# Optimization experiments

Hardware: AMD Instinct MI355X
Metric: run time of the kernel (lower is better)

Reference implementation:

```python
import jax, jax.numpy as jnp
import numpy as np
from jax import lax

HIDDEN = 256
HORIZON = 168  # 7 * 24


def _cell(x, h, c, Wih, Whh, bih, bhh):
    # PyTorch LSTM cell: gate order i, f, g, o
    gates = x @ Wih.T + bih + h @ Whh.T + bhh  # [B, 4*HIDDEN]
    i, f, g, o = jnp.split(gates, 4, axis=-1)
    c = jax.nn.sigmoid(f) * c + jax.nn.sigmoid(i) * jnp.tanh(g)
    h = jax.nn.sigmoid(o) * jnp.tanh(c)
    return h, c


def setup_inputs() -> dict:
    key = jax.random.key(0)
    ks = jax.random.split(key, 20)
    B, T, H = 1024, 336, HIDDEN
    s = 0.05

    def p(k, shape):
        return jax.random.normal(k, shape, dtype=jnp.float32) * s

    inp = {"x": jax.random.normal(ks[0], (B, T), dtype=jnp.float32)}
    # encoder layer 0 (input_size=1), layer 1 (input=HIDDEN)
    inp["enc_Wih0"] = p(ks[1], (4 * H, 1)); inp["enc_Whh0"] = p(ks[2], (4 * H, H))
    inp["enc_bih0"] = p(ks[3], (4 * H,)); inp["enc_bhh0"] = p(ks[4], (4 * H,))
    inp["enc_Wih1"] = p(ks[5], (4 * H, H)); inp["enc_Whh1"] = p(ks[6], (4 * H, H))
    inp["enc_bih1"] = p(ks[7], (4 * H,)); inp["enc_bhh1"] = p(ks[8], (4 * H,))
    # decoder layers
    inp["dec_Wih0"] = p(ks[9], (4 * H, 1)); inp["dec_Whh0"] = p(ks[10], (4 * H, H))
    inp["dec_bih0"] = p(ks[11], (4 * H,)); inp["dec_bhh0"] = p(ks[12], (4 * H,))
    inp["dec_Wih1"] = p(ks[13], (4 * H, H)); inp["dec_Whh1"] = p(ks[14], (4 * H, H))
    inp["dec_bih1"] = p(ks[15], (4 * H,)); inp["dec_bhh1"] = p(ks[16], (4 * H,))
    # final projection hidden -> 1
    inp["fc_W"] = p(ks[17], (1, H)); inp["fc_b"] = p(ks[18], (1,))
    return inp


def reference(x, enc_Wih0, enc_Whh0, enc_bih0, enc_bhh0,
              enc_Wih1, enc_Whh1, enc_bih1, enc_bhh1,
              dec_Wih0, dec_Whh0, dec_bih0, dec_bhh0,
              dec_Wih1, dec_Whh1, dec_bih1, dec_bhh1,
              fc_W, fc_b):
    B = x.shape[0]
    xs = x[:, :, None].transpose(1, 0, 2)  # [T, B, 1]
    z = jnp.zeros((B, HIDDEN), dtype=x.dtype)

    def enc_step(carry, xt):
        h0, c0, h1, c1 = carry
        h0, c0 = _cell(xt, h0, c0, enc_Wih0, enc_Whh0, enc_bih0, enc_bhh0)
        h1, c1 = _cell(h0, h1, c1, enc_Wih1, enc_Whh1, enc_bih1, enc_bhh1)
        return (h0, c0, h1, c1), None

    (h0, c0, h1, c1), _ = lax.scan(enc_step, (z, z, z, z), xs)

    dec_inp = x[:, -1:]  # [B, 1] last observed value

    def dec_step(carry, _):
        h0, c0, h1, c1, inp = carry
        h0, c0 = _cell(inp, h0, c0, dec_Wih0, dec_Whh0, dec_bih0, dec_bhh0)
        h1, c1 = _cell(h0, h1, c1, dec_Wih1, dec_Whh1, dec_bih1, dec_bhh1)
        pred = h1 @ fc_W.T + fc_b  # [B, 1]
        return (h0, c0, h1, c1, pred), pred

    _, preds = lax.scan(dec_step, (h0, c0, h1, c1, dec_inp), None, length=HORIZON)
    return preds[:, :, 0].T  # [B, HORIZON]
```

## Files before the change

### kernel.cpp

```cpp
#include <hip/hip_runtime.h>

#define HIDDEN 256
#define TENC 336
#define HORIZ 168
#define BSZ 1024
#define BH (BSZ*HIDDEN)
#define WMAT (1024*256)

typedef _Float16 f16;
typedef f16 f16x8 __attribute__((ext_vector_type(8)));
typedef float f32x4 __attribute__((ext_vector_type(4)));
typedef unsigned int u32;
typedef unsigned long long u64;

#define H0_OFF 0
#define H1_OFF (2*BH*2)
#define PP_OFF (H1_OFF + 2*BH*2)
#define FLAG_OFF (PP_OFF + BSZ*16*4)
#define WS_BASE (FLAG_OFF + 16*16*64)
#define WF16_OFF WS_BASE
#define WS_FULL (WF16_OFF + 6*WMAT*2)

#define LDS_A0 0
#define LDS_A1 32768
#define LDS_X0 65536
#define XSTRIDE 16
#define LDS_X1 (LDS_X0 + 256*XSTRIDE*4)
#define LDS_SM (LDS_X1 + 256*XSTRIDE*4)
#define LDS_TOTAL (LDS_SM + 1024)

__device__ __forceinline__ float sigm(float x){ return 1.0f/(1.0f+__expf(-x)); }
__device__ __forceinline__ float tanh_f(float x){ return 2.0f/(1.0f+__expf(-2.0f*x)) - 1.0f; }

__device__ __forceinline__ u64 ald64(const void* p){
  return __hip_atomic_load((const u64*)p, __ATOMIC_RELAXED, __HIP_MEMORY_SCOPE_AGENT);
}
__device__ __forceinline__ u32 ald32(const u32* p){
  return __hip_atomic_load(p, __ATOMIC_RELAXED, __HIP_MEMORY_SCOPE_AGENT);
}
__device__ __forceinline__ void ast32(u32* p, u32 v){
  __hip_atomic_store(p, v, __ATOMIC_RELAXED, __HIP_MEMORY_SCOPE_AGENT);
}

__device__ __forceinline__ f16x8 loadWfrag(const float* W, int grow, int k){
  const float* p = W + grow*HIDDEN + k;
  float4 lo = *(const float4*)p;
  float4 hi = *(const float4*)(p+4);
  f16x8 r;
  r[0]=(f16)lo.x; r[1]=(f16)lo.y; r[2]=(f16)lo.z; r[3]=(f16)lo.w;
  r[4]=(f16)hi.x; r[5]=(f16)hi.y; r[6]=(f16)hi.z; r[7]=(f16)hi.w;
  return r;
}

__device__ __forceinline__ const f16* slot_src(const f16* base, int g, int s){
  int l = s & 63, f = s >> 6;
  int kt = f >> 2, mt = f & 3;
  int row = g*64 + mt*16 + (l&15);
  int k = kt*32 + 8*(l>>4);
  return base + row*HIDDEN + k;
}

__device__ __forceinline__ void stage_tile(char* dst, const f16* src_base, int g, int tid){
  u64 v[8];
  #pragma unroll
  for (int i=0;i<4;++i){
    const f16* src = slot_src(src_base, g, tid + 512*i);
    v[2*i]   = ald64(src);
    v[2*i+1] = ald64(src+4);
  }
  #pragma unroll
  for (int i=0;i<4;++i){
    int s = tid + 512*i;
    *(u64*)(dst + s*16)     = v[2*i];
    *(u64*)(dst + s*16 + 8) = v[2*i+1];
  }
}

__device__ __forceinline__ void stage2(char* dA, const f16* sA, char* dB, const f16* sB,
                                       int g, int tid){
  u64 va[8], vb[8];
  #pragma unroll
  for (int i=0;i<4;++i){
    const f16* src = slot_src(sA, g, tid + 512*i);
    va[2*i]   = ald64(src);
    va[2*i+1] = ald64(src+4);
  }
  #pragma unroll
  for (int i=0;i<4;++i){
    const f16* src = slot_src(sB, g, tid + 512*i);
    vb[2*i]   = ald64(src);
    vb[2*i+1] = ald64(src+4);
  }
  #pragma unroll
  for (int i=0;i<4;++i){
    int s = tid + 512*i;
    *(u64*)(dA + s*16)     = va[2*i];
    *(u64*)(dA + s*16 + 8) = va[2*i+1];
    *(u64*)(dB + s*16)     = vb[2*i];
    *(u64*)(dB + s*16 + 8) = vb[2*i+1];
  }
}

__device__ __forceinline__ void cellpair(const float* X, const float* bs, const float* wih, float xr,
                                         int crow, int dp, float& ca, float& cb, float& hA, float& hB){
  float iA = X[(0*64+crow)*XSTRIDE+dp  ] + bs[dp]      + xr*wih[dp];
  float iB = X[(0*64+crow)*XSTRIDE+dp+1] + bs[dp+1]    + xr*wih[dp+1];
  float fA = X[(1*64+crow)*XSTRIDE+dp  ] + bs[16+dp]   + xr*wih[16+dp];
  float fB = X[(1*64+crow)*XSTRIDE+dp+1] + bs[16+dp+1] + xr*wih[16+dp+1];
  float gA = X[(2*64+crow)*XSTRIDE+dp  ] + bs[32+dp]   + xr*wih[32+dp];
  float gB = X[(2*64+crow)*XSTRIDE+dp+1] + bs[32+dp+1] + xr*wih[32+dp+1];
  float oA = X[(3*64+crow)*XSTRIDE+dp  ] + bs[48+dp]   + xr*wih[48+dp];
  float oB = X[(3*64+crow)*XSTRIDE+dp+1] + bs[48+dp+1] + xr*wih[48+dp+1];
  ca = sigm(fA)*ca + sigm(iA)*tanh_f(gA);
  cb = sigm(fB)*cb + sigm(iB)*tanh_f(gB);
  hA = sigm(oA)*tanh_f(ca);
  hB = sigm(oB)*tanh_f(cb);
}

__device__ __forceinline__ void storeh(f16* base, int rowg, int col, float hA, float hB){
  u32 pk = (u32)__builtin_bit_cast(unsigned short, (f16)hA)
         | ((u32)__builtin_bit_cast(unsigned short, (f16)hB) << 16);
  ast32((u32*)(base + rowg*HIDDEN + col), pk);
}

__device__ __forceinline__ void gbar(u32* gf, int j, int lane, int tid, u32 ev){
  __syncthreads();
  if (tid == 0) ast32(gf + j*16, ev);
  if (tid < 64 && lane < 16){
    const u32* sp = gf + lane*16;
    for (int it = 0; it < (1<<17); ++it){
      if (__all((int)(ald32(sp) >= ev))) break;
    }
  }
  __syncthreads();
}

struct P {
  const float *x;
  const float *eWih0,*eWhh0,*eBih0,*eBhh0,*eWih1,*eWhh1,*eBih1,*eBhh1;
  const float *dWih0,*dWhh0,*dBih0,*dBhh0,*dWih1,*dWhh1,*dBih1,*dBhh1;
  const float *fcW,*fcB;
  float* out;
  char* ws;
  int usef16;
};

struct WC {
  const float* src0; const float* src1; const float* src2;
  const float* src3; const float* src4; const float* src5;
  f16* dst;
};

__global__ void initk(char* ws){
  u32* p = (u32*)ws;
  size_t total = (size_t)WS_BASE / 4;
  for (size_t k = (size_t)blockIdx.x*blockDim.x + threadIdx.x; k < total;
       k += (size_t)gridDim.x*blockDim.x) p[k] = 0u;
}

__global__ void wconv(WC wc){
  int m = blockIdx.y;
  const float* s = (m==0)?wc.src0:(m==1)?wc.src1:(m==2)?wc.src2:
                   (m==3)?wc.src3:(m==4)?wc.src4:wc.src5;
  f16* d = wc.dst + (size_t)m*WMAT;
  for (int i = blockIdx.x*blockDim.x + threadIdx.x; i < WMAT;
       i += gridDim.x*blockDim.x) d[i] = (f16)s[i];
}

__global__ __launch_bounds__(512) void lstm_main(P p){
  const int tid  = threadIdx.x;
  const int lane = tid & 63;
  const int w    = tid >> 6;
  const int n    = w & 3;
  const int mh   = w >> 2;
  const int blk  = blockIdx.x;
  const int g    = blk & 15;
  const int j    = blk >> 4;

  extern __shared__ __align__(16) char smem[];
  char*  A0 = smem + LDS_A0;
  char*  A1 = smem + LDS_A1;
  float* X0 = (float*)(smem + LDS_X0);
  float* X1 = (float*)(smem + LDS_X1);
  float* wih0s = (float*)(smem + LDS_SM);
  float* b0s   = wih0s + 64;
  float* b1s   = wih0s + 128;
  float* fcWs  = wih0s + 192;
  float* fcbs  = wih0s + 208;

  f16*   h0buf = (f16*)(p.ws + H0_OFF);
  f16*   h1buf = (f16*)(p.ws + H1_OFF);
  float* ppart = (float*)(p.ws + PP_OFF);
  u32*   gf    = (u32*)(p.ws + FLAG_OFF) + g*256;
  const f16* wf = (const f16*)(p.ws + WF16_OFF);

  const int crow = tid >> 3;
  const int dp   = (tid & 7) * 2;
  const int rowg = g*64 + crow;
  const int cold = j*16 + dp;

  float c0a=0.f, c0b=0.f, c1a=0.f, c1b=0.f;

  if (tid < 64){
    int gt = tid >> 4, d = tid & 15;
    int grow = gt*256 + j*16 + d;
    wih0s[tid] = p.eWih0[grow];
    b0s[tid] = p.eBih0[grow] + p.eBhh0[grow];
    b1s[tid] = p.eBih1[grow] + p.eBhh1[grow];
  }
  if (tid < 16) fcWs[tid] = p.fcW[j*16 + tid];
  if (tid == 0) fcbs[0] = p.fcB[0];

  const int grow = n*256 + j*16 + (lane & 15);
  const int kb = 8*(lane>>4);
  f16x8 B0[8], B1i[8], B1h[8];
  if (p.usef16){
    #pragma unroll
    for (int kt=0; kt<8; ++kt){
      int ko = kt*32 + kb;
      B0[kt]  = *(const f16x8*)(wf + 0*WMAT + grow*HIDDEN + ko);
      B1i[kt] = *(const f16x8*)(wf + 1*WMAT + grow*HIDDEN + ko);
      B1h[kt] = *(const f16x8*)(wf + 2*WMAT + grow*HIDDEN + ko);
    }
  } else {
    #pragma unroll
    for (int kt=0; kt<8; ++kt){
      B0[kt]  = loadWfrag(p.eWhh0, grow, kt*32 + kb);
      B1i[kt] = loadWfrag(p.eWih1, grow, kt*32 + kb);
      B1h[kt] = loadWfrag(p.eWhh1, grow, kt*32 + kb);
    }
  }
  __syncthreads();

  u32 ev = 0;

  for (int r = 0; r <= TENC; ++r){
    float xr = (r < TENC) ? p.x[rowg*TENC + r] : 0.f;
    stage2(A0, h0buf + ((r+1)&1)*BH, A1, h1buf + (r&1)*BH, g, tid);
    __syncthreads();

    f32x4 acc0[2] = {{0.f,0.f,0.f,0.f},{0.f,0.f,0.f,0.f}};
    f32x4 acc1[2] = {{0.f,0.f,0.f,0.f},{0.f,0.f,0.f,0.f}};
    #pragma unroll
    for (int kt=0; kt<8; ++kt){
      #pragma unroll
      for (int m=0; m<2; ++m){
        f16x8 a = *(const f16x8*)(A0 + ((kt*4 + (mh*2+m))*64 + lane)*16);
        acc0[m] = __builtin_amdgcn_mfma_f32_16x16x32_f16(a, B0[kt],  acc0[m], 0,0,0);
        acc1[m] = __builtin_amdgcn_mfma_f32_16x16x32_f16(a, B1i[kt], acc1[m], 0,0,0);
      }
    }
    #pragma unroll
    for (int kt=0; kt<8; ++kt){
      #pragma unroll
      for (int m=0; m<2; ++m){
        f16x8 a = *(const f16x8*)(A1 + ((kt*4 + (mh*2+m))*64 + lane)*16);
        acc1[m] = __builtin_amdgcn_mfma_f32_16x16x32_f16(a, B1h[kt], acc1[m], 0,0,0);
      }
    }

    #pragma unroll
    for (int m=0; m<2; ++m){
      int rb = mh*32 + m*16 + 4*(lane>>4);
      #pragma unroll
      for (int q=0; q<4; ++q){
        X0[(n*64 + rb + q)*XSTRIDE + (lane&15)] = acc0[m][q];
        X1[(n*64 + rb + q)*XSTRIDE + (lane&15)] = acc1[m][q];
      }
    }
    __syncthreads();

    if (r < TENC){
      float hA, hB;
      cellpair(X0, b0s, wih0s, xr, crow, dp, c0a, c0b, hA, hB);
      storeh(h0buf + (r&1)*BH, rowg, cold, hA, hB);
    }
    if (r >= 1){
      float hA, hB;
      cellpair(X1, b1s, wih0s, 0.f, crow, dp, c1a, c1b, hA, hB);
      storeh(h1buf + ((r-1)&1)*BH, rowg, cold, hA, hB);
    }
    ++ev;
    gbar(gf, j, lane, tid, ev);
  }

  __syncthreads();
  if (tid < 64){
    int gt = tid >> 4, d = tid & 15;
    int grw = gt*256 + j*16 + d;
    wih0s[tid] = p.dWih0[grw];
    b0s[tid] = p.dBih0[grw] + p.dBhh0[grw];
    b1s[tid] = p.dBih1[grw] + p.dBhh1[grw];
  }
  if (p.usef16){
    #pragma unroll
    for (int kt=0; kt<8; ++kt){
      int ko = kt*32 + kb;
      B0[kt]  = *(const f16x8*)(wf + 3*WMAT + grow*HIDDEN + ko);
      B1i[kt] = *(const f16x8*)(wf + 4*WMAT + grow*HIDDEN + ko);
      B1h[kt] = *(const f16x8*)(wf + 5*WMAT + grow*HIDDEN + ko);
    }
  } else {
    #pragma unroll
    for (int kt=0; kt<8; ++kt){
      B0[kt]  = loadWfrag(p.dWhh0, grow, kt*32 + kb);
      B1i[kt] = loadWfrag(p.dWih1, grow, kt*32 + kb);
      B1h[kt] = loadWfrag(p.dWhh1, grow, kt*32 + kb);
    }
  }
  __syncthreads();

  for (int t = 0; t < HORIZ; ++t){
    u64 ppv = 0;
    float xlast = 0.f;
    if (t == 0) xlast = p.x[rowg*TENC + (TENC-1)];
    else        ppv   = ald64(ppart + rowg*16 + (tid&7)*2);

    stage2(A0, h0buf + ((t+1)&1)*BH, A1, h1buf + ((t+1)&1)*BH, g, tid);
    __syncthreads();

    f32x4 acc0[2] = {{0.f,0.f,0.f,0.f},{0.f,0.f,0.f,0.f}};
    f32x4 acc1[2] = {{0.f,0.f,0.f,0.f},{0.f,0.f,0.f,0.f}};
    #pragma unroll
    for (int kt=0; kt<8; ++kt){
      #pragma unroll
      for (int m=0; m<2; ++m){
        f16x8 a0 = *(const f16x8*)(A0 + ((kt*4 + (mh*2+m))*64 + lane)*16);
        acc0[m] = __builtin_amdgcn_mfma_f32_16x16x32_f16(a0, B0[kt],  acc0[m], 0,0,0);
        f16x8 a1 = *(const f16x8*)(A1 + ((kt*4 + (mh*2+m))*64 + lane)*16);
        acc1[m] = __builtin_amdgcn_mfma_f32_16x16x32_f16(a1, B1h[kt], acc1[m], 0,0,0);
      }
    }
    #pragma unroll
    for (int m=0; m<2; ++m){
      int rb = mh*32 + m*16 + 4*(lane>>4);
      #pragma unroll
      for (int q=0; q<4; ++q) X0[(n*64 + rb + q)*XSTRIDE + (lane&15)] = acc0[m][q];
    }
    __syncthreads();

    float inp;
    if (t == 0){
      inp = xlast;
    } else {
      float a = __builtin_bit_cast(float, (u32)(ppv & 0xffffffffull));
      float b = __builtin_bit_cast(float, (u32)(ppv >> 32));
      float s = a + b;
      s += __shfl_xor(s, 1);
      s += __shfl_xor(s, 2);
      s += __shfl_xor(s, 4);
      inp = s + fcbs[0];
    }
    {
      float hA, hB;
      cellpair(X0, b0s, wih0s, inp, crow, dp, c0a, c0b, hA, hB);
      storeh(h0buf + (t&1)*BH, rowg, cold, hA, hB);
    }
    if (t > 0 && j == 0 && (tid & 7) == 0) p.out[rowg*HORIZ + (t-1)] = inp;
    ++ev;
    gbar(gf, j, lane, tid, ev);

    stage_tile(A0, h0buf + (t&1)*BH, g, tid);
    __syncthreads();

    #pragma unroll
    for (int kt=0; kt<8; ++kt){
      #pragma unroll
      for (int m=0; m<2; ++m){
        f16x8 a0 = *(const f16x8*)(A0 + ((kt*4 + (mh*2+m))*64 + lane)*16);
        acc1[m] = __builtin_amdgcn_mfma_f32_16x16x32_f16(a0, B1i[kt], acc1[m], 0,0,0);
      }
    }
    #pragma unroll
    for (int m=0; m<2; ++m){
      int rb = mh*32 + m*16 + 4*(lane>>4);
      #pragma unroll
      for (int q=0; q<4; ++q) X1[(n*64 + rb + q)*XSTRIDE + (lane&15)] = acc1[m][q];
    }
    __syncthreads();

    {
      float hA, hB;
      cellpair(X1, b1s, wih0s, 0.f, crow, dp, c1a, c1b, hA, hB);
      storeh(h1buf + (t&1)*BH, rowg, cold, hA, hB);
      float pp = fcWs[dp]*hA + fcWs[dp+1]*hB;
      pp += __shfl_xor(pp, 1);
      pp += __shfl_xor(pp, 2);
      pp += __shfl_xor(pp, 4);
      if ((tid & 7) == 0)
        ast32((u32*)(ppart + rowg*16 + j), __builtin_bit_cast(u32, pp));
    }
    ++ev;
    gbar(gf, j, lane, tid, ev);
  }

  if (j == 0){
    u64 ppv = ald64(ppart + rowg*16 + (tid&7)*2);
    float a = __builtin_bit_cast(float, (u32)(ppv & 0xffffffffull));
    float b = __builtin_bit_cast(float, (u32)(ppv >> 32));
    float s = a + b;
    s += __shfl_xor(s, 1);
    s += __shfl_xor(s, 2);
    s += __shfl_xor(s, 4);
    if ((tid & 7) == 0) p.out[rowg*HORIZ + (HORIZ-1)] = s + fcbs[0];
  }
}

extern "C" void kernel_launch(void* const* d_in, const int* in_sizes, int n_in,
                              void* d_out, int out_size, void* d_ws, size_t ws_size,
                              hipStream_t stream) {
  (void)in_sizes; (void)n_in; (void)out_size;
  if (ws_size < (size_t)WS_BASE) return;
  const int usef16 = (ws_size >= (size_t)WS_FULL) ? 1 : 0;

  P prm;
  prm.x     = (const float*)d_in[0];
  prm.eWih0 = (const float*)d_in[1];  prm.eWhh0 = (const float*)d_in[2];
  prm.eBih0 = (const float*)d_in[3];  prm.eBhh0 = (const float*)d_in[4];
  prm.eWih1 = (const float*)d_in[5];  prm.eWhh1 = (const float*)d_in[6];
  prm.eBih1 = (const float*)d_in[7];  prm.eBhh1 = (const float*)d_in[8];
  prm.dWih0 = (const float*)d_in[9];  prm.dWhh0 = (const float*)d_in[10];
  prm.dBih0 = (const float*)d_in[11]; prm.dBhh0 = (const float*)d_in[12];
  prm.dWih1 = (const float*)d_in[13]; prm.dWhh1 = (const float*)d_in[14];
  prm.dBih1 = (const float*)d_in[15]; prm.dBhh1 = (const float*)d_in[16];
  prm.fcW   = (const float*)d_in[17]; prm.fcB   = (const float*)d_in[18];
  prm.out   = (float*)d_out;
  prm.ws    = (char*)d_ws;
  prm.usef16 = usef16;

  hipLaunchKernelGGL(initk, dim3(256), dim3(256), 0, stream, (char*)d_ws);

  if (usef16){
    WC wc;
    wc.src0 = prm.eWhh0; wc.src1 = prm.eWih1; wc.src2 = prm.eWhh1;
    wc.src3 = prm.dWhh0; wc.src4 = prm.dWih1; wc.src5 = prm.dWhh1;
    wc.dst  = (f16*)((char*)d_ws + WF16_OFF);
    hipLaunchKernelGGL(wconv, dim3(128, 6), dim3(256), 0, stream, wc);
  }

  hipFuncSetAttribute((const void*)lstm_main,
                      hipFuncAttributeMaxDynamicSharedMemorySize, LDS_TOTAL);
  void* args[] = { &prm };
  hipLaunchCooperativeKernel((const void*)lstm_main, dim3(256), dim3(512),
                             args, LDS_TOTAL, stream);
}
```

Before: 4.385 ms.

## Split group barrier into per-layer flag signals to overlap layer pipelines

Replaces the single per-group barrier with two flag arrays, one for layer-0 and one for layer-1 hidden-state readiness, each signalled and polled separately. In the encoder, a block can start layer-0 work as soon as the previous layer-0 states are published, without waiting on layer-1 completion, which lets the two layers' stages skew and overlap across blocks. In exchange there are more polling points per step and subtler ordering requirements (flag counts, WAR hazards on double-buffered h) that could cause races if any dependency is missing. The poll timeout is raised.

```diff
diff --git a/kernel.cpp b/kernel.cpp
--- a/kernel.cpp
+++ b/kernel.cpp
@@ -17,7 +17,7 @@
 #define H1_OFF (2*BH*2)
 #define PP_OFF (H1_OFF + 2*BH*2)
 #define FLAG_OFF (PP_OFF + BSZ*16*4)
-#define WS_BASE (FLAG_OFF + 16*16*64)
+#define WS_BASE (FLAG_OFF + 16*32*64)
 #define WF16_OFF WS_BASE
 #define WS_FULL (WF16_OFF + 6*WMAT*2)
 
@@ -123,16 +123,22 @@
   ast32((u32*)(base + rowg*HIDDEN + col), pk);
 }
 
-__device__ __forceinline__ void gbar(u32* gf, int j, int lane, int tid, u32 ev){
+__device__ __forceinline__ void pollw(const u32* f0, u32 t0, const u32* f1, u32 t1, int tid){
+  if (tid < 64){
+    const u32* sp = nullptr; u32 tgt = 0;
+    if (tid < 16){ sp = f0 + tid*16; tgt = t0; }
+    else if (f1 != nullptr && tid < 32){ sp = f1 + (tid-16)*16; tgt = t1; }
+    for (int it = 0; it < (1<<20); ++it){
+      bool ok = (sp == nullptr) || (ald32(sp) >= tgt);
+      if (__all((int)ok)) break;
+    }
+  }
   __syncthreads();
-  if (tid == 0) ast32(gf + j*16, ev);
-  if (tid < 64 && lane < 16){
-    const u32* sp = gf + lane*16;
-    for (int it = 0; it < (1<<17); ++it){
-      if (__all((int)(ald32(sp) >= ev))) break;
-    }
-  }
+}
+
+__device__ __forceinline__ void sigf(u32* line, u32 v, int tid){
   __syncthreads();
+  if (tid == 0) ast32(line, v);
 }
 
 struct P {
@@ -191,8 +197,11 @@
   f16*   h0buf = (f16*)(p.ws + H0_OFF);
   f16*   h1buf = (f16*)(p.ws + H1_OFF);
   float* ppart = (float*)(p.ws + PP_OFF);
-  u32*   gf    = (u32*)(p.ws + FLAG_OFF) + g*256;
-  const f16* wf = (const f16*)(p.ws + WF16_OFF);
+  u32*   sfb   = (u32*)(p.ws + FLAG_OFF);
+  u32*   p0    = sfb + (g*32 + 0 )*16;
+  u32*   p1    = sfb + (g*32 + 16)*16;
+  u32*   my0   = p0 + j*16;
+  u32*   my1   = p1 + j*16;
 
   const int crow = tid >> 3;
   const int dp   = (tid & 7) * 2;
@@ -203,10 +212,10 @@
 
   if (tid < 64){
     int gt = tid >> 4, d = tid & 15;
-    int grow = gt*256 + j*16 + d;
-    wih0s[tid] = p.eWih0[grow];
-    b0s[tid] = p.eBih0[grow] + p.eBhh0[grow];
-    b1s[tid] = p.eBih1[grow] + p.eBhh1[grow];
+    int grw = gt*256 + j*16 + d;
+    wih0s[tid] = p.eWih0[grw];
+    b0s[tid] = p.eBih0[grw] + p.eBhh0[grw];
+    b1s[tid] = p.eBih1[grw] + p.eBhh1[grw];
   }
   if (tid < 16) fcWs[tid] = p.fcW[j*16 + tid];
   if (tid == 0) fcbs[0] = p.fcB[0];
@@ -214,6 +223,7 @@
   const int grow = n*256 + j*16 + (lane & 15);
   const int kb = 8*(lane>>4);
   f16x8 B0[8], B1i[8], B1h[8];
+  const f16* wf = (const f16*)(p.ws + WF16_OFF);
   if (p.usef16){
     #pragma unroll
     for (int kt=0; kt<8; ++kt){
@@ -232,11 +242,11 @@
   }
   __syncthreads();
 
-  u32 ev = 0;
-
   for (int r = 0; r <= TENC; ++r){
     float xr = (r < TENC) ? p.x[rowg*TENC + r] : 0.f;
-    stage2(A0, h0buf + ((r+1)&1)*BH, A1, h1buf + (r&1)*BH, g, tid);
+
+    pollw(p0, (u32)r, nullptr, 0, tid);
+    stage_tile(A0, h0buf + ((r+1)&1)*BH, g, tid);
     __syncthreads();
 
     f32x4 acc0[2] = {{0.f,0.f,0.f,0.f},{0.f,0.f,0.f,0.f}};
@@ -251,6 +261,25 @@
       }
     }
     #pragma unroll
+    for (int m=0; m<2; ++m){
+      int rb = mh*32 + m*16 + 4*(lane>>4);
+      #pragma unroll
+      for (int q=0; q<4; ++q) X0[(n*64 + rb + q)*XSTRIDE + (lane&15)] = acc0[m][q];
+    }
+    __syncthreads();
+
+    if (r < TENC){
+      float hA, hB;
+      cellpair(X0, b0s, wih0s, xr, crow, dp, c0a, c0b, hA, hB);
+      storeh(h0buf + (r&1)*BH, rowg, cold, hA, hB);
+    }
+    sigf(my0, (u32)(r+1), tid);
+
+    pollw(p1, (u32)r, nullptr, 0, tid);
+    stage_tile(A1, h1buf + (r&1)*BH, g, tid);
+    __syncthreads();
+
+    #pragma unroll
     for (int kt=0; kt<8; ++kt){
       #pragma unroll
       for (int m=0; m<2; ++m){
@@ -258,30 +287,20 @@
         acc1[m] = __builtin_amdgcn_mfma_f32_16x16x32_f16(a, B1h[kt], acc1[m], 0,0,0);
       }
     }
-
     #pragma unroll
     for (int m=0; m<2; ++m){
       int rb = mh*32 + m*16 + 4*(lane>>4);
       #pragma unroll
-      for (int q=0; q<4; ++q){
-        X0[(n*64 + rb + q)*XSTRIDE + (lane&15)] = acc0[m][q];
-        X1[(n*64 + rb + q)*XSTRIDE + (lane&15)] = acc1[m][q];
-      }
-    }
-    __syncthreads();
-
-    if (r < TENC){
-      float hA, hB;
-      cellpair(X0, b0s, wih0s, xr, crow, dp, c0a, c0b, hA, hB);
-      storeh(h0buf + (r&1)*BH, rowg, cold, hA, hB);
-    }
+      for (int q=0; q<4; ++q) X1[(n*64 + rb + q)*XSTRIDE + (lane&15)] = acc1[m][q];
+    }
+    __syncthreads();
+
     if (r >= 1){
       float hA, hB;
       cellpair(X1, b1s, wih0s, 0.f, crow, dp, c1a, c1b, hA, hB);
       storeh(h1buf + ((r-1)&1)*BH, rowg, cold, hA, hB);
     }
-    ++ev;
-    gbar(gf, j, lane, tid, ev);
+    sigf(my1, (u32)(r+1), tid);
   }
 
   __syncthreads();
@@ -311,6 +330,9 @@
   __syncthreads();
 
   for (int t = 0; t < HORIZ; ++t){
+    const u32 base = 337u + (u32)t;
+
+    pollw(p0, base, p1, base, tid);
     u64 ppv = 0;
     float xlast = 0.f;
     if (t == 0) xlast = p.x[rowg*TENC + (TENC-1)];
@@ -357,9 +379,9 @@
       storeh(h0buf + (t&1)*BH, rowg, cold, hA, hB);
     }
     if (t > 0 && j == 0 && (tid & 7) == 0) p.out[rowg*HORIZ + (t-1)] = inp;
-    ++ev;
-    gbar(gf, j, lane, tid, ev);
-
+    sigf(my0, base+1u, tid);
+
+    pollw(p0, base+1u, nullptr, 0, tid);
     stage_tile(A0, h0buf + (t&1)*BH, g, tid);
     __syncthreads();
 
@@ -390,11 +412,11 @@
       if ((tid & 7) == 0)
         ast32((u32*)(ppart + rowg*16 + j), __builtin_bit_cast(u32, pp));
     }
-    ++ev;
-    gbar(gf, j, lane, tid, ev);
+    sigf(my1, base+1u, tid);
   }
 
   if (j == 0){
+    pollw(p1, 337u + (u32)HORIZ, nullptr, 0, tid);
     u64 ppv = ald64(ppart + rowg*16 + (tid&7)*2);
     float a = __builtin_bit_cast(float, (u32)(ppv & 0xffffffffull));
     float b = __builtin_bit_cast(float, (u32)(ppv >> 32));
```

Result: faster. 4.289 ms (-2.2%).
